# Performance work log

Measured on AMD Instinct MI355X. Metric: run time of the kernel, lower is better.

The kernel has to match this reference:

```python
import jax, jax.numpy as jnp
import numpy as np

B, S, HID = 2, 2048, 1024
NH = 16
HD = HID // NH  # 64
ROPE_BASE = 10000.0


def _rope_cos_sin(seq_len, head_dim, dtype):
    inv_freq = 1.0 / (ROPE_BASE ** (jnp.arange(0, head_dim, 2, dtype=jnp.float32) / head_dim))
    t = jnp.arange(seq_len, dtype=jnp.float32)
    freqs = jnp.einsum('s,d->sd', t, inv_freq)            # [S, HD/2]
    emb = jnp.concatenate([freqs, freqs], axis=-1)        # [S, HD]
    return jnp.cos(emb).astype(dtype), jnp.sin(emb).astype(dtype)


def _rotate_half(x):
    x1, x2 = jnp.split(x, 2, axis=-1)
    return jnp.concatenate([-x2, x1], axis=-1)


def setup_inputs() -> dict:
    key = jax.random.key(0)
    k1, k2, k3, k4 = jax.random.split(key, 4)
    hidden_states = jax.random.normal(k1, (B, S, HID), dtype=jnp.float32)
    scale_in = 1.0 / np.sqrt(HID)
    w_qkv = jax.random.normal(k2, (HID, 3 * HID), dtype=jnp.float32) * scale_in
    w_dense = jax.random.normal(k3, (HID, HID), dtype=jnp.float32) * scale_in
    b_dense = jax.random.normal(k4, (HID,), dtype=jnp.float32) * 0.01
    return {"hidden_states": hidden_states, "w_qkv": w_qkv,
            "w_dense": w_dense, "b_dense": b_dense}


def reference(hidden_states, w_qkv, w_dense, b_dense):
    b, s, _ = hidden_states.shape
    # Fused QKV projection (no bias), split into q, k, v of [B, S, HID] each.
    fused = hidden_states @ w_qkv                           # [B, S, 3*HID]
    q, k, v = jnp.split(fused, 3, axis=-1)
    # [B, S, NH, HD] -> [B, NH, S, HD]
    q = q.reshape(b, s, NH, HD).transpose(0, 2, 1, 3)
    k = k.reshape(b, s, NH, HD).transpose(0, 2, 1, 3)
    v = v.reshape(b, s, NH, HD).transpose(0, 2, 1, 3)
    # Rotary position embedding on q and k.
    cos, sin = _rope_cos_sin(s, HD, hidden_states.dtype)    # [S, HD]
    cos = cos[None, None, :, :]
    sin = sin[None, None, :, :]
    q = q * cos + _rotate_half(q) * sin
    k = k * cos + _rotate_half(k) * sin
    # Naive causal attention with full score materialization.
    inv_norm = 1.0 / jnp.sqrt(jnp.asarray(HD, dtype=hidden_states.dtype))
    scores = jnp.einsum('bhqd,bhkd->bhqk', q, k) * inv_norm  # [B, NH, S, S]
    causal = jnp.tril(jnp.ones((s, s), dtype=bool))[None, None, :, :]
    neg = jnp.asarray(jnp.finfo(scores.dtype).min, dtype=scores.dtype)
    scores = jnp.where(causal, scores, neg)
    attn = jax.nn.softmax(scores, axis=-1)
    out = jnp.einsum('bhqk,bhkd->bhqd', attn, v)            # [B, NH, S, HD]
    out = out.transpose(0, 2, 1, 3).reshape(b, s, HID)
    return out @ w_dense + b_dense
```

## Files before the change

kernel.cpp:

```cpp
#include <hip/hip_runtime.h>

#define B_ 2
#define S_ 2048
#define HID_ 1024
#define NH_ 16
#define HD_ 64

typedef _Float16 half8 __attribute__((ext_vector_type(8)));
typedef float f32x4 __attribute__((ext_vector_type(4)));

__device__ __forceinline__ void gload16(const _Float16* g, _Float16* l) {
    __builtin_amdgcn_global_load_lds(
        (const __attribute__((address_space(1))) void*)g,
        (__attribute__((address_space(3))) void*)l, 16, 0, 0);
}


__global__ void k_cast_f32_f16(const float* __restrict__ in, _Float16* __restrict__ out, int n) {
    int i = (blockIdx.x * blockDim.x + threadIdx.x) * 8;
    if (i >= n) return;
    float4 a = *(const float4*)&in[i];
    float4 b = *(const float4*)&in[i + 4];
    half8 h;
    h[0] = (_Float16)a.x; h[1] = (_Float16)a.y; h[2] = (_Float16)a.z; h[3] = (_Float16)a.w;
    h[4] = (_Float16)b.x; h[5] = (_Float16)b.y; h[6] = (_Float16)b.z; h[7] = (_Float16)b.w;
    *(half8*)&out[i] = h;
}

__global__ void k_transpose_cast(const float* __restrict__ in, _Float16* __restrict__ out,
                                 int K, int N) {
    __shared__ float tile[32][33];
    int n0 = blockIdx.x * 32, k0 = blockIdx.y * 32;
    int tx = threadIdx.x, ty = threadIdx.y;
    #pragma unroll
    for (int i = 0; i < 32; i += 8)
        tile[ty + i][tx] = in[(size_t)(k0 + ty + i) * N + n0 + tx];
    __syncthreads();
    #pragma unroll
    for (int i = 0; i < 32; i += 8)
        out[(size_t)(n0 + ty + i) * K + k0 + tx] = (_Float16)tile[tx][ty + i];
}

__global__ void k_rope_tables(float* __restrict__ cos_t, float* __restrict__ sin_t) {
    int s = blockIdx.x;
    int i = threadIdx.x;
    float inv = powf(10000.0f, -(float)(2 * i) / 64.0f);
    float ang = (float)s * inv;
    cos_t[s * 32 + i] = cosf(ang);
    sin_t[s * 32 + i] = sinf(ang);
}

__global__ __launch_bounds__(256) void k_reshape_rope(
        const _Float16* __restrict__ fused, const float* __restrict__ cos_t,
        const float* __restrict__ sin_t, _Float16* __restrict__ qh,
        _Float16* __restrict__ kh, _Float16* __restrict__ vt) {
    int blk = blockIdx.x;
    int s0 = (blk & 31) * 64;
    int bh = blk >> 5;
    int h = bh & 15;
    int t = threadIdx.x;
    int r = t >> 2, dq0 = (t & 3) * 16;
    int s = s0 + r;
    const _Float16* fr = fused + ((size_t)(bh >> 4) * S_ + s) * 3072;
    size_t qkbase = ((size_t)bh * S_ + s) * HD_;
    int pq0 = dq0 ^ 32;
    float sgn = (dq0 < 32) ? -1.f : 1.f;

    half8 qm[2], qp[2], km[2], kp[2], vm[2];
    qm[0] = *(const half8*)&fr[h * 64 + dq0];
    qm[1] = *(const half8*)&fr[h * 64 + dq0 + 8];
    qp[0] = *(const half8*)&fr[h * 64 + pq0];
    qp[1] = *(const half8*)&fr[h * 64 + pq0 + 8];
    km[0] = *(const half8*)&fr[1024 + h * 64 + dq0];
    km[1] = *(const half8*)&fr[1024 + h * 64 + dq0 + 8];
    kp[0] = *(const half8*)&fr[1024 + h * 64 + pq0];
    kp[1] = *(const half8*)&fr[1024 + h * 64 + pq0 + 8];
    vm[0] = *(const half8*)&fr[2048 + h * 64 + dq0];
    vm[1] = *(const half8*)&fr[2048 + h * 64 + dq0 + 8];

    const float* cb = &cos_t[s * 32 + (dq0 & 31)];
    const float* sb = &sin_t[s * 32 + (dq0 & 31)];
    half8 qo[2], ko[2];
    #pragma unroll
    for (int v8 = 0; v8 < 2; ++v8)
        #pragma unroll
        for (int j = 0; j < 8; ++j) {
            float cs = cb[v8 * 8 + j], sn = sb[v8 * 8 + j];
            qo[v8][j] = (_Float16)((float)qm[v8][j] * cs + sgn * (float)qp[v8][j] * sn);
            ko[v8][j] = (_Float16)((float)km[v8][j] * cs + sgn * (float)kp[v8][j] * sn);
        }
    *(half8*)&qh[qkbase + dq0]     = qo[0];
    *(half8*)&qh[qkbase + dq0 + 8] = qo[1];
    *(half8*)&kh[qkbase + dq0]     = ko[0];
    *(half8*)&kh[qkbase + dq0 + 8] = ko[1];

    __shared__ _Float16 vtile[64][80];
    *(half8*)&vtile[r][dq0]     = vm[0];
    *(half8*)&vtile[r][dq0 + 8] = vm[1];
    __syncthreads();
    int dd = t >> 2, sc0 = (t & 3) * 16;
    _Float16 vv[16];
    #pragma unroll
    for (int j = 0; j < 16; ++j)
        vv[j] = vtile[sc0 + j][dd];
    size_t vbase = ((size_t)bh * HD_ + dd) * (size_t)S_ + s0 + sc0;
    *(half8*)&vt[vbase]     = *(half8*)&vv[0];
    *(half8*)&vt[vbase + 8] = *(half8*)&vv[8];
}

template <bool WRITE_F32>
__global__ __launch_bounds__(256) void k_gemm(const _Float16* __restrict__ A,
                                              const _Float16* __restrict__ Bt,
                                              void* __restrict__ Cout,
                                              const float* __restrict__ bias,
                                              int M, int N, int K) {
    __shared__ _Float16 At[128 * 32];
    __shared__ _Float16 Bts[128 * 32];
    int t = threadIdx.x;
    int nb = N >> 7;
    int nwg = (M >> 7) * nb;
    int bid = blockIdx.x;
    int swz = (bid & 7) * (nwg >> 3) + (bid >> 3);
    int m0 = (swz / nb) << 7;
    int n0 = (swz % nb) << 7;
    int lane = t & 63, wid = t >> 6;
    int wm = (wid >> 1) * 64, wn = (wid & 1) * 64;
    int lr = lane & 15, lg = lane >> 4;
    f32x4 acc[4][4] = {};
    for (int k0 = 0; k0 < K; k0 += 32) {
        __syncthreads();
        #pragma unroll
        for (int it = 0; it < 2; ++it) {
            int idx = it * 256 + t;
            int row = idx >> 2, c = (idx & 3) * 8;
            gload16(&A[(size_t)(m0 + row) * K + k0 + c], &At[idx * 8]);
            gload16(&Bt[(size_t)(n0 + row) * K + k0 + c], &Bts[idx * 8]);
        }
        __syncthreads();
        half8 af[4], bf[4];
        #pragma unroll
        for (int i = 0; i < 4; ++i)
            af[i] = *(const half8*)&At[(wm + i * 16 + lr) * 32 + lg * 8];
        #pragma unroll
        for (int i = 0; i < 4; ++i)
            bf[i] = *(const half8*)&Bts[(wn + i * 16 + lr) * 32 + lg * 8];
        #pragma unroll
        for (int i = 0; i < 4; ++i)
            #pragma unroll
            for (int j = 0; j < 4; ++j)
                acc[i][j] = __builtin_amdgcn_mfma_f32_16x16x32_f16(af[i], bf[j], acc[i][j], 0, 0, 0);
    }
    #pragma unroll
    for (int i = 0; i < 4; ++i) {
        #pragma unroll
        for (int j = 0; j < 4; ++j) {
            #pragma unroll
            for (int r2 = 0; r2 < 4; ++r2) {
                int row = m0 + wm + i * 16 + lg * 4 + r2;
                int col = n0 + wn + j * 16 + lr;
                float v = acc[i][j][r2];
                if constexpr (WRITE_F32)
                    ((float*)Cout)[(size_t)row * N + col] = v + bias[col];
                else
                    ((_Float16*)Cout)[(size_t)row * N + col] = (_Float16)v;
            }
        }
    }
}

__global__ __launch_bounds__(256) void k_attn(const _Float16* __restrict__ qh,
                                              const _Float16* __restrict__ kh,
                                              const _Float16* __restrict__ vt,
                                              _Float16* __restrict__ attn_out) {
    int blk0 = blockIdx.x;
    int x = blk0 & 7;
    int i = blk0 >> 3;
    int bh = x * 4 + (i >> 4);
    int p = i & 15;
    int qtA = p, qtB = 31 - p;
    int t = threadIdx.x, lane = t & 63, w = t >> 6;
    int lr = lane & 15, lg = lane >> 4;
    const _Float16* Qb = qh + (size_t)bh * S_ * HD_;
    const _Float16* Kb = kh + (size_t)bh * S_ * HD_;
    const _Float16* Vb = vt + (size_t)bh * HD_ * S_;

    __shared__ _Float16 Kt[2][64 * 64];
    __shared__ _Float16 Vt[2][64 * 64];
    __shared__ _Float16 Pl[4][16 * 64];

    const _Float16 qsc = (_Float16)0.18033688f;
    half8 qfA[2], qfB[2];
    {
        int qA = qtA * 64 + w * 16 + lr;
        int qB = qtB * 64 + w * 16 + lr;
        #pragma unroll
        for (int dh = 0; dh < 2; ++dh) {
            qfA[dh] = *(const half8*)&Qb[(size_t)qA * 64 + dh * 32 + lg * 8];
            qfB[dh] = *(const half8*)&Qb[(size_t)qB * 64 + dh * 32 + lg * 8];
            #pragma unroll
            for (int j = 0; j < 8; ++j) { qfA[dh][j] *= qsc; qfB[dh][j] *= qsc; }
        }
    }

    f32x4 accA[4] = {}, accB[4] = {};
    float mA = -1e30f, lA = 0.f, mB = -1e30f, lB = 0.f;
    int swq = lr & 7;
    int s0 = 0, cur = 0;

    auto STAGE = [&](int bsel, int s0s) {
        #pragma unroll
        for (int cc = 0; cc < 2; ++cc) {
            int base = w * 128 + cc * 64;
            int idx = base + lane;
            int row = idx >> 3;
            int cg = (idx & 7) ^ (row & 7);
            gload16(&Kb[(size_t)(s0s + row) * 64 + cg * 8], &Kt[bsel][base * 8]);
            gload16(&Vb[(size_t)row * S_ + s0s + cg * 8], &Vt[bsel][base * 8]);
        }
    };

    auto process = [&](const half8* qf, f32x4* acc, float& mrun, float& lrun, int q0g) {
        int qw0 = q0g + w * 16;
        int q = qw0 + lr;
        f32x4 sc[4];
        #pragma unroll
        for (int nt = 0; nt < 4; ++nt) {
            int rr = nt * 16 + lr;
            half8 kf0 = *(const half8*)&Kt[cur][rr * 64 + ((lg ^ swq) * 8)];
            half8 kf1 = *(const half8*)&Kt[cur][rr * 64 + (((4 + lg) ^ swq) * 8)];
            f32x4 z = {0.f, 0.f, 0.f, 0.f};
            z = __builtin_amdgcn_mfma_f32_16x16x32_f16(kf0, qf[0], z, 0, 0, 0);
            z = __builtin_amdgcn_mfma_f32_16x16x32_f16(kf1, qf[1], z, 0, 0, 0);
            sc[nt] = z;
        }
        if (s0 + 64 > qw0) {
            #pragma unroll
            for (int nt = 0; nt < 4; ++nt)
                #pragma unroll
                for (int r = 0; r < 4; ++r) {
                    int kv = s0 + nt * 16 + lg * 4 + r;
                    if (kv > q) sc[nt][r] = -1e30f;
                }
        }
        float mx = sc[0][0];
        #pragma unroll
        for (int nt = 0; nt < 4; ++nt)
            #pragma unroll
            for (int r = 0; r < 4; ++r) mx = fmaxf(mx, sc[nt][r]);
        mx = fmaxf(mx, __shfl_xor(mx, 16));
        mx = fmaxf(mx, __shfl_xor(mx, 32));

        if (!__all(mx <= mrun + 11.f)) {
            float mnew = fmaxf(mrun, mx);
            float fac = __builtin_amdgcn_exp2f(mrun - mnew);
            mrun = mnew;
            lrun *= fac;
            float facv[4];
            #pragma unroll
            for (int r = 0; r < 4; ++r) facv[r] = __shfl(fac, lg * 4 + r);
            #pragma unroll
            for (int dt = 0; dt < 4; ++dt)
                #pragma unroll
                for (int r = 0; r < 4; ++r) acc[dt][r] *= facv[r];
        }

        float rs = 0.f;
        #pragma unroll
        for (int nt = 0; nt < 4; ++nt)
            #pragma unroll
            for (int r = 0; r < 4; ++r) {
                float pv = __builtin_amdgcn_exp2f(sc[nt][r] - mrun);
                sc[nt][r] = pv;
                rs += pv;
            }
        rs += __shfl_xor(rs, 16);
        rs += __shfl_xor(rs, 32);
        lrun += rs;

        #pragma unroll
        for (int nt = 0; nt < 4; ++nt) {
            unsigned ua = __builtin_bit_cast(unsigned, __builtin_amdgcn_cvt_pkrtz(sc[nt][0], sc[nt][1]));
            unsigned ub = __builtin_bit_cast(unsigned, __builtin_amdgcn_cvt_pkrtz(sc[nt][2], sc[nt][3]));
            int chunk = 2 * nt + (lg >> 1);
            char* pp = (char*)&Pl[w][0] + lr * 128 + ((chunk ^ swq) * 16) + (lg & 1) * 8;
            *(uint2*)pp = make_uint2(ua, ub);
        }
        half8 pa[2];
        #pragma unroll
        for (int hh = 0; hh < 2; ++hh)
            pa[hh] = *(const half8*)((const char*)&Pl[w][0] + lr * 128 + (((4 * hh + lg) ^ swq) * 16));

        #pragma unroll
        for (int dt = 0; dt < 4; ++dt) {
            int vr = dt * 16 + lr;
            #pragma unroll
            for (int hh = 0; hh < 2; ++hh) {
                half8 vb = *(const half8*)&Vt[cur][vr * 64 + (((4 * hh + lg) ^ swq) * 8)];
                acc[dt] = __builtin_amdgcn_mfma_f32_16x16x32_f16(pa[hh], vb, acc[dt], 0, 0, 0);
            }
        }
    };

    int ntiles = qtB + 1;
    STAGE(0, 0);
    for (int ti = 0; ti < ntiles; ++ti) {
        s0 = ti << 6;
        cur = ti & 1;
        __syncthreads();
        if (ti + 1 < ntiles) STAGE(cur ^ 1, s0 + 64);
        process(qfB, accB, mB, lB, qtB * 64);
        if (ti <= qtA)
            process(qfA, accA, mA, lA, qtA * 64);
    }

    int b = bh >> 4, h = bh & 15;
    auto writeout = [&](const f32x4* acc, float lrun, int q0g) {
        float linv[4];
        #pragma unroll
        for (int r = 0; r < 4; ++r) linv[r] = 1.0f / __shfl(lrun, lg * 4 + r);
        #pragma unroll
        for (int dt = 0; dt < 4; ++dt)
            #pragma unroll
            for (int r = 0; r < 4; ++r) {
                int s = q0g + w * 16 + lg * 4 + r;
                attn_out[((size_t)b * S_ + s) * HID_ + h * 64 + dt * 16 + lr] =
                    (_Float16)(acc[dt][r] * linv[r]);
            }
    };
    writeout(accB, lB, qtB * 64);
    writeout(accA, lA, qtA * 64);
}


extern "C" void kernel_launch(void* const* d_in, const int* in_sizes, int n_in,
                              void* d_out, int out_size, void* d_ws, size_t ws_size,
                              hipStream_t stream) {
    const float* hidden  = (const float*)d_in[0];
    const float* w_qkv   = (const float*)d_in[1];
    const float* w_dense = (const float*)d_in[2];
    const float* b_dense = (const float*)d_in[3];
    float* out = (float*)d_out;
    char* ws = (char*)d_ws;

    _Float16* hh     = (_Float16*)(ws + 0);
    _Float16* wqkvT  = (_Float16*)(ws + 8388608);
    _Float16* wdT    = (_Float16*)(ws + 14680064);
    float*    cos_t  = (float*)   (ws + 16777216);
    float*    sin_t  = (float*)   (ws + 17039360);
    _Float16* fused  = (_Float16*)(ws + 17301504);
    _Float16* kh     = (_Float16*)(ws + 42467328);
    _Float16* vt     = (_Float16*)(ws + 50855936);
    _Float16* qh     = hh;
    _Float16* attn_o = fused;

    k_cast_f32_f16<<<2048, 256, 0, stream>>>(hidden, hh, B_ * S_ * HID_);
    k_transpose_cast<<<dim3(3 * HID_ / 32, HID_ / 32), dim3(32, 8), 0, stream>>>(w_qkv, wqkvT, HID_, 3 * HID_);
    k_transpose_cast<<<dim3(HID_ / 32, HID_ / 32), dim3(32, 8), 0, stream>>>(w_dense, wdT, HID_, HID_);
    k_rope_tables<<<S_, 32, 0, stream>>>(cos_t, sin_t);

    k_gemm<false><<<(B_ * S_ / 128) * (3 * HID_ / 128), 256, 0, stream>>>(
        hh, wqkvT, (void*)fused, nullptr, B_ * S_, 3 * HID_, HID_);

    k_reshape_rope<<<B_ * NH_ * (S_ / 64), 256, 0, stream>>>(fused, cos_t, sin_t, qh, kh, vt);

    k_attn<<<B_ * NH_ * (S_ / 64) / 2, 256, 0, stream>>>(qh, kh, vt, attn_o);

    k_gemm<true><<<(B_ * S_ / 128) * (HID_ / 128), 256, 0, stream>>>(
        attn_o, wdT, (void*)out, b_dense, B_ * S_, HID_, HID_);
}
```

Before: 208.6 us.

## Merge prep kernels into one launch and interleave dual-tile attention MFMAs

```diff
diff --git a/kernel.cpp b/kernel.cpp
--- a/kernel.cpp
+++ b/kernel.cpp
@@ -16,38 +16,48 @@
 }
 
 
-__global__ void k_cast_f32_f16(const float* __restrict__ in, _Float16* __restrict__ out, int n) {
-    int i = (blockIdx.x * blockDim.x + threadIdx.x) * 8;
-    if (i >= n) return;
-    float4 a = *(const float4*)&in[i];
-    float4 b = *(const float4*)&in[i + 4];
-    half8 h;
-    h[0] = (_Float16)a.x; h[1] = (_Float16)a.y; h[2] = (_Float16)a.z; h[3] = (_Float16)a.w;
-    h[4] = (_Float16)b.x; h[5] = (_Float16)b.y; h[6] = (_Float16)b.z; h[7] = (_Float16)b.w;
-    *(half8*)&out[i] = h;
-}
-
-__global__ void k_transpose_cast(const float* __restrict__ in, _Float16* __restrict__ out,
-                                 int K, int N) {
-    __shared__ float tile[32][33];
-    int n0 = blockIdx.x * 32, k0 = blockIdx.y * 32;
-    int tx = threadIdx.x, ty = threadIdx.y;
+__device__ __forceinline__ void tr32(const float* __restrict__ in, _Float16* __restrict__ out,
+                                     int K, int N, int n0, int k0, int tx, int ty,
+                                     float (*tile)[33]) {
     #pragma unroll
-    for (int i = 0; i < 32; i += 8)
-        tile[ty + i][tx] = in[(size_t)(k0 + ty + i) * N + n0 + tx];
+    for (int i2 = 0; i2 < 32; i2 += 8)
+        tile[ty + i2][tx] = in[(size_t)(k0 + ty + i2) * N + n0 + tx];
     __syncthreads();
     #pragma unroll
-    for (int i = 0; i < 32; i += 8)
-        out[(size_t)(n0 + ty + i) * K + k0 + tx] = (_Float16)tile[tx][ty + i];
-}
-
-__global__ void k_rope_tables(float* __restrict__ cos_t, float* __restrict__ sin_t) {
-    int s = blockIdx.x;
-    int i = threadIdx.x;
-    float inv = powf(10000.0f, -(float)(2 * i) / 64.0f);
-    float ang = (float)s * inv;
-    cos_t[s * 32 + i] = cosf(ang);
-    sin_t[s * 32 + i] = sinf(ang);
+    for (int i2 = 0; i2 < 32; i2 += 8)
+        out[(size_t)(n0 + ty + i2) * K + k0 + tx] = (_Float16)tile[tx][ty + i2];
+}
+
+__global__ __launch_bounds__(256) void k_prep(
+        const float* __restrict__ hidden, const float* __restrict__ w_qkv,
+        const float* __restrict__ w_dense, _Float16* __restrict__ hh,
+        _Float16* __restrict__ wqkvT, _Float16* __restrict__ wdT,
+        float* __restrict__ cos_t, float* __restrict__ sin_t) {
+    int b = blockIdx.x, t = threadIdx.x;
+    __shared__ float tile[32][33];
+    if (b < 2048) {
+        int i = (b * 256 + t) * 8;
+        float4 a = *(const float4*)&hidden[i];
+        float4 c = *(const float4*)&hidden[i + 4];
+        half8 h;
+        h[0] = (_Float16)a.x; h[1] = (_Float16)a.y; h[2] = (_Float16)a.z; h[3] = (_Float16)a.w;
+        h[4] = (_Float16)c.x; h[5] = (_Float16)c.y; h[6] = (_Float16)c.z; h[7] = (_Float16)c.w;
+        *(half8*)&hh[i] = h;
+    } else if (b < 5120) {
+        int bb = b - 2048;
+        tr32(w_qkv, wqkvT, HID_, 3 * HID_, (bb % 96) * 32, (bb / 96) * 32, t & 31, t >> 5, tile);
+    } else if (b < 6144) {
+        int bb = b - 5120;
+        tr32(w_dense, wdT, HID_, HID_, (bb % 32) * 32, (bb / 32) * 32, t & 31, t >> 5, tile);
+    } else {
+        int bb = b - 6144;
+        int s = bb * 8 + (t >> 5);
+        int ii = t & 31;
+        float inv = powf(10000.0f, -(float)(2 * ii) / 64.0f);
+        float ang = (float)s * inv;
+        cos_t[s * 32 + ii] = cosf(ang);
+        sin_t[s * 32 + ii] = sinf(ang);
+    }
 }
 
 __global__ __launch_bounds__(256) void k_reshape_rope(
@@ -186,7 +196,8 @@
 
     __shared__ _Float16 Kt[2][64 * 64];
     __shared__ _Float16 Vt[2][64 * 64];
-    __shared__ _Float16 Pl[4][16 * 64];
+    __shared__ _Float16 PlB[4][16 * 64];
+    __shared__ _Float16 PlA[4][16 * 64];
 
     const _Float16 qsc = (_Float16)0.18033688f;
     half8 qfA[2], qfB[2];
@@ -219,34 +230,24 @@
         }
     };
 
-    auto process = [&](const half8* qf, f32x4* acc, float& mrun, float& lrun, int q0g) {
+    auto smax = [&](f32x4 (&z)[4], float& mrun, float& lrun, f32x4 (&acc)[4],
+                    _Float16* plw, bool domask, int q0g, half8 (&pa)[2]) {
         int qw0 = q0g + w * 16;
-        int q = qw0 + lr;
-        f32x4 sc[4];
-        #pragma unroll
-        for (int nt = 0; nt < 4; ++nt) {
-            int rr = nt * 16 + lr;
-            half8 kf0 = *(const half8*)&Kt[cur][rr * 64 + ((lg ^ swq) * 8)];
-            half8 kf1 = *(const half8*)&Kt[cur][rr * 64 + (((4 + lg) ^ swq) * 8)];
-            f32x4 z = {0.f, 0.f, 0.f, 0.f};
-            z = __builtin_amdgcn_mfma_f32_16x16x32_f16(kf0, qf[0], z, 0, 0, 0);
-            z = __builtin_amdgcn_mfma_f32_16x16x32_f16(kf1, qf[1], z, 0, 0, 0);
-            sc[nt] = z;
-        }
-        if (s0 + 64 > qw0) {
+        if (domask) {
+            int q = qw0 + lr;
             #pragma unroll
             for (int nt = 0; nt < 4; ++nt)
                 #pragma unroll
                 for (int r = 0; r < 4; ++r) {
                     int kv = s0 + nt * 16 + lg * 4 + r;
-                    if (kv > q) sc[nt][r] = -1e30f;
+                    if (kv > q) z[nt][r] = -1e30f;
                 }
         }
-        float mx = sc[0][0];
+        float mx = z[0][0];
         #pragma unroll
         for (int nt = 0; nt < 4; ++nt)
             #pragma unroll
-            for (int r = 0; r < 4; ++r) mx = fmaxf(mx, sc[nt][r]);
+            for (int r = 0; r < 4; ++r) mx = fmaxf(mx, z[nt][r]);
         mx = fmaxf(mx, __shfl_xor(mx, 16));
         mx = fmaxf(mx, __shfl_xor(mx, 32));
 
@@ -269,8 +270,8 @@
         for (int nt = 0; nt < 4; ++nt)
             #pragma unroll
             for (int r = 0; r < 4; ++r) {
-                float pv = __builtin_amdgcn_exp2f(sc[nt][r] - mrun);
-                sc[nt][r] = pv;
+                float pv = __builtin_amdgcn_exp2f(z[nt][r] - mrun);
+                z[nt][r] = pv;
                 rs += pv;
             }
         rs += __shfl_xor(rs, 16);
@@ -279,38 +280,85 @@
 
         #pragma unroll
         for (int nt = 0; nt < 4; ++nt) {
-            unsigned ua = __builtin_bit_cast(unsigned, __builtin_amdgcn_cvt_pkrtz(sc[nt][0], sc[nt][1]));
-            unsigned ub = __builtin_bit_cast(unsigned, __builtin_amdgcn_cvt_pkrtz(sc[nt][2], sc[nt][3]));
+            unsigned ua = __builtin_bit_cast(unsigned, __builtin_amdgcn_cvt_pkrtz(z[nt][0], z[nt][1]));
+            unsigned ub = __builtin_bit_cast(unsigned, __builtin_amdgcn_cvt_pkrtz(z[nt][2], z[nt][3]));
             int chunk = 2 * nt + (lg >> 1);
-            char* pp = (char*)&Pl[w][0] + lr * 128 + ((chunk ^ swq) * 16) + (lg & 1) * 8;
+            char* pp = (char*)plw + lr * 128 + ((chunk ^ swq) * 16) + (lg & 1) * 8;
             *(uint2*)pp = make_uint2(ua, ub);
         }
-        half8 pa[2];
         #pragma unroll
         for (int hh = 0; hh < 2; ++hh)
-            pa[hh] = *(const half8*)((const char*)&Pl[w][0] + lr * 128 + (((4 * hh + lg) ^ swq) * 16));
-
-        #pragma unroll
-        for (int dt = 0; dt < 4; ++dt) {
-            int vr = dt * 16 + lr;
-            #pragma unroll
-            for (int hh = 0; hh < 2; ++hh) {
-                half8 vb = *(const half8*)&Vt[cur][vr * 64 + (((4 * hh + lg) ^ swq) * 8)];
-                acc[dt] = __builtin_amdgcn_mfma_f32_16x16x32_f16(pa[hh], vb, acc[dt], 0, 0, 0);
-            }
-        }
+            pa[hh] = *(const half8*)((const char*)plw + lr * 128 + (((4 * hh + lg) ^ swq) * 16));
     };
 
-    int ntiles = qtB + 1;
     STAGE(0, 0);
-    for (int ti = 0; ti < ntiles; ++ti) {
+    for (int ti = 0; ti <= qtB; ++ti) {
         s0 = ti << 6;
         cur = ti & 1;
         __syncthreads();
-        if (ti + 1 < ntiles) STAGE(cur ^ 1, s0 + 64);
-        process(qfB, accB, mB, lB, qtB * 64);
-        if (ti <= qtA)
-            process(qfA, accA, mA, lA, qtA * 64);
+        if (ti < qtB) STAGE(cur ^ 1, s0 + 64);
+
+        if (ti <= qtA) {
+            f32x4 zB[4], zA[4];
+            __builtin_amdgcn_s_setprio(1);
+            #pragma unroll
+            for (int nt = 0; nt < 4; ++nt) {
+                int rr = nt * 16 + lr;
+                half8 kf0 = *(const half8*)&Kt[cur][rr * 64 + ((lg ^ swq) * 8)];
+                half8 kf1 = *(const half8*)&Kt[cur][rr * 64 + (((4 + lg) ^ swq) * 8)];
+                f32x4 z = {0.f, 0.f, 0.f, 0.f};
+                z = __builtin_amdgcn_mfma_f32_16x16x32_f16(kf0, qfB[0], z, 0, 0, 0);
+                z = __builtin_amdgcn_mfma_f32_16x16x32_f16(kf1, qfB[1], z, 0, 0, 0);
+                zB[nt] = z;
+                f32x4 y = {0.f, 0.f, 0.f, 0.f};
+                y = __builtin_amdgcn_mfma_f32_16x16x32_f16(kf0, qfA[0], y, 0, 0, 0);
+                y = __builtin_amdgcn_mfma_f32_16x16x32_f16(kf1, qfA[1], y, 0, 0, 0);
+                zA[nt] = y;
+            }
+            __builtin_amdgcn_s_setprio(0);
+            half8 paB[2], paA[2];
+            smax(zB, mB, lB, accB, &PlB[w][0], false, qtB * 64, paB);
+            smax(zA, mA, lA, accA, &PlA[w][0], ti == qtA, qtA * 64, paA);
+            __builtin_amdgcn_s_setprio(1);
+            #pragma unroll
+            for (int dt = 0; dt < 4; ++dt) {
+                int vr = dt * 16 + lr;
+                #pragma unroll
+                for (int hh = 0; hh < 2; ++hh) {
+                    half8 vb = *(const half8*)&Vt[cur][vr * 64 + (((4 * hh + lg) ^ swq) * 8)];
+                    accB[dt] = __builtin_amdgcn_mfma_f32_16x16x32_f16(paB[hh], vb, accB[dt], 0, 0, 0);
+                    accA[dt] = __builtin_amdgcn_mfma_f32_16x16x32_f16(paA[hh], vb, accA[dt], 0, 0, 0);
+                }
+            }
+            __builtin_amdgcn_s_setprio(0);
+        } else {
+            f32x4 zB[4];
+            __builtin_amdgcn_s_setprio(1);
+            #pragma unroll
+            for (int nt = 0; nt < 4; ++nt) {
+                int rr = nt * 16 + lr;
+                half8 kf0 = *(const half8*)&Kt[cur][rr * 64 + ((lg ^ swq) * 8)];
+                half8 kf1 = *(const half8*)&Kt[cur][rr * 64 + (((4 + lg) ^ swq) * 8)];
+                f32x4 z = {0.f, 0.f, 0.f, 0.f};
+                z = __builtin_amdgcn_mfma_f32_16x16x32_f16(kf0, qfB[0], z, 0, 0, 0);
+                z = __builtin_amdgcn_mfma_f32_16x16x32_f16(kf1, qfB[1], z, 0, 0, 0);
+                zB[nt] = z;
+            }
+            __builtin_amdgcn_s_setprio(0);
+            half8 paB[2];
+            smax(zB, mB, lB, accB, &PlB[w][0], ti == qtB, qtB * 64, paB);
+            __builtin_amdgcn_s_setprio(1);
+            #pragma unroll
+            for (int dt = 0; dt < 4; ++dt) {
+                int vr = dt * 16 + lr;
+                #pragma unroll
+                for (int hh = 0; hh < 2; ++hh) {
+                    half8 vb = *(const half8*)&Vt[cur][vr * 64 + (((4 * hh + lg) ^ swq) * 8)];
+                    accB[dt] = __builtin_amdgcn_mfma_f32_16x16x32_f16(paB[hh], vb, accB[dt], 0, 0, 0);
+                }
+            }
+            __builtin_amdgcn_s_setprio(0);
+        }
     }
 
     int b = bh >> 4, h = bh & 15;
@@ -353,10 +401,7 @@
     _Float16* qh     = hh;
     _Float16* attn_o = fused;
 
-    k_cast_f32_f16<<<2048, 256, 0, stream>>>(hidden, hh, B_ * S_ * HID_);
-    k_transpose_cast<<<dim3(3 * HID_ / 32, HID_ / 32), dim3(32, 8), 0, stream>>>(w_qkv, wqkvT, HID_, 3 * HID_);
-    k_transpose_cast<<<dim3(HID_ / 32, HID_ / 32), dim3(32, 8), 0, stream>>>(w_dense, wdT, HID_, HID_);
-    k_rope_tables<<<S_, 32, 0, stream>>>(cos_t, sin_t);
+    k_prep<<<6400, 256, 0, stream>>>(hidden, w_qkv, w_dense, hh, wqkvT, wdT, cos_t, sin_t);
 
     k_gemm<false><<<(B_ * S_ / 128) * (3 * HID_ / 128), 256, 0, stream>>>(
         hh, wqkvT, (void*)fused, nullptr, B_ * S_, 3 * HID_, HID_);
```

Result: no change. 205.0 us (-1.7%).
